# Optimization experiments

Hardware: AMD Instinct MI355X
Metric: run time of the kernel (lower is better)

## Reference

```python
import jax, jax.numpy as jnp
import numpy as np

B = 1024      # batch
E = 1024      # encoding_dim
OUT = 34      # 17 joints x 2 coords


def setup_inputs() -> dict:
    key = jax.random.key(0)
    ks = jax.random.split(key, 8)
    s = 0.02  # weight init scale
    return {
        "h": jax.random.normal(ks[0], (B, E), dtype=jnp.float32),
        "c": jax.random.normal(ks[1], (B, E), dtype=jnp.float32),
        "W_ih": jax.random.normal(ks[2], (4 * E, E), dtype=jnp.float32) * s,
        "W_hh": jax.random.normal(ks[3], (4 * E, E), dtype=jnp.float32) * s,
        "b_ih": jax.random.normal(ks[4], (4 * E,), dtype=jnp.float32) * s,
        "b_hh": jax.random.normal(ks[5], (4 * E,), dtype=jnp.float32) * s,
        "W_out": jax.random.normal(ks[6], (OUT, E), dtype=jnp.float32) * s,
        "b_out": jax.random.normal(ks[7], (OUT,), dtype=jnp.float32) * s,
        "future_preds": 10,
    }


def reference(h, c, W_ih, W_hh, b_ih, b_hh, W_out, b_out, future_preds):
    E_ = h.shape[1]
    start = jnp.zeros_like(h)  # zeros=True start token

    def step(carry, _):
        h_t, c_t, x = carry
        # LSTMCell: gates in PyTorch order i, f, g, o
        gates = x @ W_ih.T + b_ih + h_t @ W_hh.T + b_hh  # [B, 4E]
        i = jax.nn.sigmoid(gates[:, 0 * E_:1 * E_])
        f = jax.nn.sigmoid(gates[:, 1 * E_:2 * E_])
        g = jnp.tanh(gates[:, 2 * E_:3 * E_])
        o = jax.nn.sigmoid(gates[:, 3 * E_:4 * E_])
        c_new = f * c_t + i * g
        h_new = o * jnp.tanh(c_new)
        return (h_new, c_new, h_new), h_new

    _, hs = jax.lax.scan(step, (h, c, start), None, length=future_preds)
    # hs: [T, B, E] -> [B, T, E]
    preds = jnp.transpose(hs, (1, 0, 2))
    return preds @ W_out.T + b_out  # [B, T, 34]
```

## Files before the change

kernel.cpp:

```cpp
#include <hip/hip_runtime.h>
#include <cstdint>
#include <cstddef>

#define E_DIM   1024
#define B_DIM   1024
#define HPITCH  1040
#define T_STEPS 10
#define OUT_DIM 34
#define OUT_PAD 48
#define HSTR    24
#define QK      256
#define WQ_ELEMS (64 * QK)
#define DYN_LDS (2 * WQ_ELEMS * 2 + 128 * HSTR * 2)
#define HSLOT  ((size_t)B_DIM * HPITCH)

typedef __attribute__((ext_vector_type(4))) float  f32x4;
typedef __attribute__((ext_vector_type(8))) __bf16 bf16x8;

__device__ __forceinline__ unsigned short f2bf(float f) {
    unsigned int u = __float_as_uint(f);
    u = (u + 0x7FFFu + ((u >> 16) & 1u)) >> 16;
    return (unsigned short)u;
}
__device__ __forceinline__ float sigmoid_(float x) { return 1.0f / (1.0f + __expf(-x)); }
__device__ __forceinline__ float tanh_(float x)    { return 2.0f / (1.0f + __expf(-2.0f * x)) - 1.0f; }

__global__ void prep_weights_frag(const float* __restrict__ W_ih, const float* __restrict__ W_hh,
                                  unsigned short* __restrict__ WsumF, unsigned short* __restrict__ WhhF) {
    const int bn = blockIdx.x >> 3, qtr = (blockIdx.x >> 1) & 3, half = blockIdx.x & 1;
    const int nt = threadIdx.x >> 6, lane = threadIdx.x & 63;
    const int j = lane & 15, q = lane >> 4;
    const int srow = nt * E_DIM + bn * 16 + j;
    const float* wi = W_ih + (size_t)srow * E_DIM;
    const float* wh = W_hh + (size_t)srow * E_DIM;
    const size_t dstb = (size_t)bn * 65536 + (size_t)qtr * 16384 + nt * 512 + lane * 8;
#pragma unroll
    for (int ks8i = 0; ks8i < 4; ++ks8i) {
        const int ks8 = half * 4 + ks8i;
        const int k = qtr * 256 + ks8 * 32 + q * 8;
        float4 i0 = *(const float4*)(wi + k);
        float4 i1 = *(const float4*)(wi + k + 4);
        float4 h0 = *(const float4*)(wh + k);
        float4 h1 = *(const float4*)(wh + k + 4);
        unsigned short* ds = WsumF + dstb + ks8 * 2048;
        unsigned short* dh = WhhF  + dstb + ks8 * 2048;
        ds[0] = f2bf(i0.x + h0.x); ds[1] = f2bf(i0.y + h0.y);
        ds[2] = f2bf(i0.z + h0.z); ds[3] = f2bf(i0.w + h0.w);
        ds[4] = f2bf(i1.x + h1.x); ds[5] = f2bf(i1.y + h1.y);
        ds[6] = f2bf(i1.z + h1.z); ds[7] = f2bf(i1.w + h1.w);
        dh[0] = f2bf(h0.x); dh[1] = f2bf(h0.y); dh[2] = f2bf(h0.z); dh[3] = f2bf(h0.w);
        dh[4] = f2bf(h1.x); dh[5] = f2bf(h1.y); dh[6] = f2bf(h1.z); dh[7] = f2bf(h1.w);
    }
}

__global__ void prep_state(const float* __restrict__ h0, const float* __restrict__ c0,
                           const float* __restrict__ W_out,
                           const float* __restrict__ b_ih, const float* __restrict__ b_hh,
                           unsigned short* __restrict__ hbuf, unsigned short* __restrict__ Woutp,
                           float* __restrict__ bperm, float* __restrict__ C) {
    const int b = blockIdx.x;
    const int t = threadIdx.x;
    if (b < 1024) {
        const size_t src = ((size_t)b * 256 + t) * 4;
        float4 hv = *(const float4*)(h0 + src);
        const size_t i = (size_t)b * HPITCH + t * 4;
        hbuf[i + 0] = f2bf(hv.x);
        hbuf[i + 1] = f2bf(hv.y);
        hbuf[i + 2] = f2bf(hv.z);
        hbuf[i + 3] = f2bf(hv.w);
    } else if (b < 1072) {
        const int o = b - 1024;
        const int k = t * 4;
        float4 w = make_float4(0.f, 0.f, 0.f, 0.f);
        if (o < OUT_DIM) w = *(const float4*)(W_out + (size_t)o * E_DIM + k);
        const size_t dst = (size_t)o * E_DIM + k;
        Woutp[dst + 0] = f2bf(w.x);
        Woutp[dst + 1] = f2bf(w.y);
        Woutp[dst + 2] = f2bf(w.z);
        Woutp[dst + 3] = f2bf(w.w);
    } else if (b < 1088) {
        const int n = (b - 1072) * 256 + t;
        const int g = (n >> 4) & 3;
        const int e = ((n >> 6) << 4) | (n & 15);
        const int srow = g * E_DIM + e;
        bperm[n] = b_ih[srow] + b_hh[srow];
    } else {
        const int m = b - 1088;
        const int e0 = t * 4;
        float4 v = *(const float4*)(c0 + (size_t)m * E_DIM + e0);
        const int bm = m >> 7, wave = (m >> 5) & 3, mt = (m >> 4) & 1, q = (m >> 2) & 3, r = m & 3;
        const float vv[4] = {v.x, v.y, v.z, v.w};
#pragma unroll
        for (int ii = 0; ii < 4; ++ii) {
            const int e = e0 + ii;
            const int bn = e >> 4, jj = e & 15;
            const int lane = q * 16 + jj;
            C[(((size_t)(bn * 8 + bm) * 4 + wave) * 64 + lane) * 8 + mt * 4 + r] = vv[ii];
        }
    }
}

__global__ __launch_bounds__(256, 2) void lstm_step(
    const unsigned short* __restrict__ WF,
    const float* __restrict__ bp,
    const unsigned short* __restrict__ Hin,
    float* __restrict__ C,
    unsigned short* __restrict__ Hout)
{
    extern __shared__ __align__(16) unsigned short smem[];
    unsigned short* Wbuf0 = smem;
    unsigned short* Wbuf1 = smem + WQ_ELEMS;
    unsigned short* Ht    = smem + 2 * WQ_ELEMS;

    const int tid  = threadIdx.x;
    const int wave = tid >> 6;
    const int lane = tid & 63;
    const int bn = blockIdx.x;
    const int bm = blockIdx.y;
    const int j  = lane & 15;
    const int q  = lane >> 4;

    f32x4 acc[2][4];
#pragma unroll
    for (int a = 0; a < 2; ++a)
#pragma unroll
        for (int b = 0; b < 4; ++b) acc[a][b] = (f32x4){0.f, 0.f, 0.f, 0.f};

    const int nb = bn * 64 + j;
    const float bi = bp[nb +  0];
    const float bf = bp[nb + 16];
    const float bg = bp[nb + 32];
    const float bo = bp[nb + 48];
    const size_t cbase = (((size_t)(bn * 8 + bm) * 4 + wave) * 64 + lane) * 8;
    float4 cold0 = *(const float4*)(C + cbase);
    float4 cold1 = *(const float4*)(C + cbase + 4);

    const unsigned short* arow0 = Hin + (size_t)(bm * 128 + wave * 32 + j) * HPITCH + q * 8;
    const unsigned short* arow1 = arow0 + (size_t)16 * HPITCH;
    const unsigned short* wsrc  = WF + (size_t)bn * 65536;

    uint4 ra[8][2];
#pragma unroll
    for (int p = 0; p < 8; ++p) {
        ra[p][0] = *(const uint4*)(arow0 + p * 32);
        ra[p][1] = *(const uint4*)(arow1 + p * 32);
    }

    uint4 wreg[8];
#pragma unroll
    for (int i = 0; i < 8; ++i)
        wreg[i] = *(const uint4*)(wsrc + (i * 256 + tid) * 8);
#pragma unroll
    for (int i = 0; i < 8; ++i)
        *(uint4*)(Wbuf0 + (i * 256 + tid) * 8) = wreg[i];
    __syncthreads();

    for (int qtr = 0; qtr < 4; ++qtr) {
        if (qtr < 3) {
#pragma unroll
            for (int i = 0; i < 8; ++i)
                wreg[i] = *(const uint4*)(wsrc + (size_t)(qtr + 1) * WQ_ELEMS + (i * 256 + tid) * 8);
        }
        const unsigned short* wb = ((qtr & 1) ? Wbuf1 : Wbuf0) + lane * 8;
#pragma unroll
        for (int ks8 = 0; ks8 < 8; ++ks8) {
            const int ks = qtr * 8 + ks8;
            bf16x8 av0 = __builtin_bit_cast(bf16x8, ra[ks8][0]);
            bf16x8 av1 = __builtin_bit_cast(bf16x8, ra[ks8][1]);
            bf16x8 bv[4];
#pragma unroll
            for (int nt = 0; nt < 4; ++nt)
                bv[nt] = *(const bf16x8*)(wb + (ks8 * 4 + nt) * 512);
#pragma unroll
            for (int nt = 0; nt < 4; ++nt) {
                acc[0][nt] = __builtin_amdgcn_mfma_f32_16x16x32_bf16(av0, bv[nt], acc[0][nt], 0, 0, 0);
                acc[1][nt] = __builtin_amdgcn_mfma_f32_16x16x32_bf16(av1, bv[nt], acc[1][nt], 0, 0, 0);
            }
            if (ks < 24) {
                ra[ks8][0] = *(const uint4*)(arow0 + (ks + 8) * 32);
                ra[ks8][1] = *(const uint4*)(arow1 + (ks + 8) * 32);
            }
        }
        if (qtr < 3) {
            unsigned short* wn_ = ((qtr + 1) & 1) ? Wbuf1 : Wbuf0;
#pragma unroll
            for (int i = 0; i < 8; ++i)
                *(uint4*)(wn_ + (i * 256 + tid) * 8) = wreg[i];
            __syncthreads();
        }
    }

    float4 cnew[2];
    const float coldv[2][4] = {{cold0.x, cold0.y, cold0.z, cold0.w},
                               {cold1.x, cold1.y, cold1.z, cold1.w}};
#pragma unroll
    for (int mt = 0; mt < 2; ++mt) {
#pragma unroll
        for (int r = 0; r < 4; ++r) {
            const float iv = sigmoid_(acc[mt][0][r] + bi);
            const float fv = sigmoid_(acc[mt][1][r] + bf);
            const float gv = tanh_(acc[mt][2][r] + bg);
            const float ov = sigmoid_(acc[mt][3][r] + bo);
            const float cn = fv * coldv[mt][r] + iv * gv;
            cnew[mt][r] = cn;
            const int rowl = wave * 32 + mt * 16 + q * 4 + r;
            Ht[rowl * HSTR + j] = f2bf(ov * tanh_(cn));
        }
    }
    *(float4*)(C + cbase)     = cnew[0];
    *(float4*)(C + cbase + 4) = cnew[1];
    __syncthreads();

    {
        const int row = tid >> 1, part = tid & 1;
        uint4 v = *(const uint4*)(Ht + row * HSTR + part * 8);
        *(uint4*)(Hout + (size_t)(bm * 128 + row) * HPITCH + bn * 16 + part * 8) = v;
    }
}

__global__ __launch_bounds__(256) void proj_kernel(
    const unsigned short* __restrict__ Hs,
    const unsigned short* __restrict__ Wo,
    const float* __restrict__ b_out,
    float* __restrict__ Out)
{
    __shared__ float red[4][32][OUT_PAD];

    const int tid = threadIdx.x, wave = tid >> 6, lane = tid & 63;
    const int j = lane & 15, q = lane >> 4;
    const int t  = blockIdx.y;
    const int bb = blockIdx.x;
    const unsigned short* Hbase = Hs + (size_t)t * HSLOT + (size_t)bb * 32 * HPITCH;
    const int k0 = wave * 256;

    f32x4 acc[2][3];
#pragma unroll
    for (int a = 0; a < 2; ++a)
#pragma unroll
        for (int b = 0; b < 3; ++b) acc[a][b] = (f32x4){0.f, 0.f, 0.f, 0.f};

#pragma unroll
    for (int kk = 0; kk < 256; kk += 32) {
        const int kc = k0 + kk + q * 8;
        bf16x8 av[2], bv[3];
#pragma unroll
        for (int mt = 0; mt < 2; ++mt)
            av[mt] = *(const bf16x8*)(Hbase + (size_t)(mt * 16 + j) * HPITCH + kc);
#pragma unroll
        for (int nt = 0; nt < 3; ++nt)
            bv[nt] = *(const bf16x8*)(Wo + (size_t)(nt * 16 + j) * E_DIM + kc);
#pragma unroll
        for (int mt = 0; mt < 2; ++mt)
#pragma unroll
            for (int nt = 0; nt < 3; ++nt)
                acc[mt][nt] = __builtin_amdgcn_mfma_f32_16x16x32_bf16(av[mt], bv[nt], acc[mt][nt], 0, 0, 0);
    }

#pragma unroll
    for (int mt = 0; mt < 2; ++mt)
#pragma unroll
        for (int nt = 0; nt < 3; ++nt)
#pragma unroll
            for (int r = 0; r < 4; ++r)
                red[wave][mt * 16 + q * 4 + r][nt * 16 + j] = acc[mt][nt][r];
    __syncthreads();

#pragma unroll
    for (int ii = 0; ii < 6; ++ii) {
        const int idx = tid * 6 + ii;
        const int row = idx / OUT_PAD, o = idx % OUT_PAD;
        if (o < OUT_DIM) {
            const float s = red[0][row][o] + red[1][row][o] + red[2][row][o] + red[3][row][o];
            Out[((size_t)(bb * 32 + row) * T_STEPS + t) * OUT_DIM + o] = s + b_out[o];
        }
    }
}

extern "C" void kernel_launch(void* const* d_in, const int* in_sizes, int n_in,
                              void* d_out, int out_size, void* d_ws, size_t ws_size,
                              hipStream_t stream) {
    (void)in_sizes; (void)n_in; (void)out_size; (void)ws_size;
    const float* h     = (const float*)d_in[0];
    const float* c     = (const float*)d_in[1];
    const float* W_ih  = (const float*)d_in[2];
    const float* W_hh  = (const float*)d_in[3];
    const float* b_ih  = (const float*)d_in[4];
    const float* b_hh  = (const float*)d_in[5];
    const float* W_out = (const float*)d_in[6];
    const float* b_out = (const float*)d_in[7];
    float* out = (float*)d_out;

    char* ws = (char*)d_ws;
    unsigned short* WsumF = (unsigned short*)(ws + 0);
    unsigned short* WhhF  = (unsigned short*)(ws + 8388608);
    float*          bperm = (float*)(ws + 16777216);
    unsigned short* Woutp = (unsigned short*)(ws + 16842752);
    float*          cbuf  = (float*)(ws + 16941056);
    unsigned short* hs    = (unsigned short*)(ws + 21135360);

    hipFuncSetAttribute((const void*)lstm_step,
                        hipFuncAttributeMaxDynamicSharedMemorySize, DYN_LDS);

    prep_weights_frag<<<512, 256, 0, stream>>>(W_ih, W_hh, WsumF, WhhF);
    prep_state<<<2112, 256, 0, stream>>>(h, c, W_out, b_ih, b_hh, hs, Woutp, bperm, cbuf);

    lstm_step<<<dim3(64, 8), 256, DYN_LDS, stream>>>(WhhF, bperm, hs, cbuf, hs + HSLOT);
    for (int t = 1; t < T_STEPS; ++t)
        lstm_step<<<dim3(64, 8), 256, DYN_LDS, stream>>>(WsumF, bperm,
                                                         hs + (size_t)t * HSLOT,
                                                         cbuf,
                                                         hs + (size_t)(t + 1) * HSLOT);

    proj_kernel<<<dim3(32, T_STEPS), 256, 0, stream>>>(hs + HSLOT, Woutp, b_out, out);
}
```

Measured before the change: 284.0 us.

## Load full weight slice into LDS once per 512-thread block covering 256 rows

Each block now has 512 threads and covers 256 batch rows instead of 128, so the grid halves. The block loads the whole 64-column weight slice (128 KB bf16) into LDS once, replacing the quarter-wise double buffering with its per-quarter barriers. Each weight slice is now read from global memory by half as many blocks, and three syncs per block go away. In exchange LDS use per block rises to about 140 KB, the upfront load is no longer overlapped with MFMA work, and occupancy likely drops to one block per CU.

```diff
diff --git a/kernel.cpp b/kernel.cpp
--- a/kernel.cpp
+++ b/kernel.cpp
@@ -9,9 +9,9 @@
 #define OUT_DIM 34
 #define OUT_PAD 48
 #define HSTR    24
-#define QK      256
-#define WQ_ELEMS (64 * QK)
-#define DYN_LDS (2 * WQ_ELEMS * 2 + 128 * HSTR * 2)
+#define WSLICE  65536
+#define HT_ROWS 256
+#define DYN_LDS (WSLICE * 2 + HT_ROWS * HSTR * 2)
 #define HSLOT  ((size_t)B_DIM * HPITCH)
 
 typedef __attribute__((ext_vector_type(4))) float  f32x4;
@@ -100,7 +100,7 @@
     }
 }
 
-__global__ __launch_bounds__(256, 2) void lstm_step(
+__global__ __launch_bounds__(512, 2) void lstm_step(
     const unsigned short* __restrict__ WF,
     const float* __restrict__ bp,
     const unsigned short* __restrict__ Hin,
@@ -108,15 +108,14 @@
     unsigned short* __restrict__ Hout)
 {
     extern __shared__ __align__(16) unsigned short smem[];
-    unsigned short* Wbuf0 = smem;
-    unsigned short* Wbuf1 = smem + WQ_ELEMS;
-    unsigned short* Ht    = smem + 2 * WQ_ELEMS;
+    unsigned short* Wlds = smem;
+    unsigned short* Ht   = smem + WSLICE;
 
     const int tid  = threadIdx.x;
-    const int wave = tid >> 6;
+    const int w    = tid >> 6;
     const int lane = tid & 63;
     const int bn = blockIdx.x;
-    const int bm = blockIdx.y;
+    const int g  = blockIdx.y;
     const int j  = lane & 15;
     const int q  = lane >> 4;
 
@@ -131,13 +130,27 @@
     const float bf = bp[nb + 16];
     const float bg = bp[nb + 32];
     const float bo = bp[nb + 48];
-    const size_t cbase = (((size_t)(bn * 8 + bm) * 4 + wave) * 64 + lane) * 8;
+    const int obm = g * 2 + (w >> 2), owv = w & 3;
+    const size_t cbase = (((size_t)(bn * 8 + obm) * 4 + owv) * 64 + lane) * 8;
     float4 cold0 = *(const float4*)(C + cbase);
     float4 cold1 = *(const float4*)(C + cbase + 4);
 
-    const unsigned short* arow0 = Hin + (size_t)(bm * 128 + wave * 32 + j) * HPITCH + q * 8;
+    const unsigned short* arow0 = Hin + (size_t)(g * 256 + w * 32 + j) * HPITCH + q * 8;
     const unsigned short* arow1 = arow0 + (size_t)16 * HPITCH;
-    const unsigned short* wsrc  = WF + (size_t)bn * 65536;
+    const unsigned short* wsrc  = WF + (size_t)bn * WSLICE;
+
+    {
+        uint4 wreg[8];
+#pragma unroll
+        for (int r2 = 0; r2 < 2; ++r2) {
+#pragma unroll
+            for (int i = 0; i < 8; ++i)
+                wreg[i] = *(const uint4*)(wsrc + ((r2 * 8 + i) * 512 + tid) * 8);
+#pragma unroll
+            for (int i = 0; i < 8; ++i)
+                *(uint4*)(Wlds + ((r2 * 8 + i) * 512 + tid) * 8) = wreg[i];
+        }
+    }
 
     uint4 ra[8][2];
 #pragma unroll
@@ -145,23 +158,10 @@
         ra[p][0] = *(const uint4*)(arow0 + p * 32);
         ra[p][1] = *(const uint4*)(arow1 + p * 32);
     }
-
-    uint4 wreg[8];
-#pragma unroll
-    for (int i = 0; i < 8; ++i)
-        wreg[i] = *(const uint4*)(wsrc + (i * 256 + tid) * 8);
-#pragma unroll
-    for (int i = 0; i < 8; ++i)
-        *(uint4*)(Wbuf0 + (i * 256 + tid) * 8) = wreg[i];
     __syncthreads();
 
     for (int qtr = 0; qtr < 4; ++qtr) {
-        if (qtr < 3) {
-#pragma unroll
-            for (int i = 0; i < 8; ++i)
-                wreg[i] = *(const uint4*)(wsrc + (size_t)(qtr + 1) * WQ_ELEMS + (i * 256 + tid) * 8);
-        }
-        const unsigned short* wb = ((qtr & 1) ? Wbuf1 : Wbuf0) + lane * 8;
+        const unsigned short* wb = Wlds + qtr * 16384 + lane * 8;
 #pragma unroll
         for (int ks8 = 0; ks8 < 8; ++ks8) {
             const int ks = qtr * 8 + ks8;
@@ -181,13 +181,6 @@
                 ra[ks8][1] = *(const uint4*)(arow1 + (ks + 8) * 32);
             }
         }
-        if (qtr < 3) {
-            unsigned short* wn_ = ((qtr + 1) & 1) ? Wbuf1 : Wbuf0;
-#pragma unroll
-            for (int i = 0; i < 8; ++i)
-                *(uint4*)(wn_ + (i * 256 + tid) * 8) = wreg[i];
-            __syncthreads();
-        }
     }
 
     float4 cnew[2];
@@ -203,7 +196,7 @@
             const float ov = sigmoid_(acc[mt][3][r] + bo);
             const float cn = fv * coldv[mt][r] + iv * gv;
             cnew[mt][r] = cn;
-            const int rowl = wave * 32 + mt * 16 + q * 4 + r;
+            const int rowl = w * 32 + mt * 16 + q * 4 + r;
             Ht[rowl * HSTR + j] = f2bf(ov * tanh_(cn));
         }
     }
@@ -214,7 +207,7 @@
     {
         const int row = tid >> 1, part = tid & 1;
         uint4 v = *(const uint4*)(Ht + row * HSTR + part * 8);
-        *(uint4*)(Hout + (size_t)(bm * 128 + row) * HPITCH + bn * 16 + part * 8) = v;
+        *(uint4*)(Hout + (size_t)(g * 256 + row) * HPITCH + bn * 16 + part * 8) = v;
     }
 }
 
@@ -304,9 +297,9 @@
     prep_weights_frag<<<512, 256, 0, stream>>>(W_ih, W_hh, WsumF, WhhF);
     prep_state<<<2112, 256, 0, stream>>>(h, c, W_out, b_ih, b_hh, hs, Woutp, bperm, cbuf);
 
-    lstm_step<<<dim3(64, 8), 256, DYN_LDS, stream>>>(WhhF, bperm, hs, cbuf, hs + HSLOT);
+    lstm_step<<<dim3(64, 4), 512, DYN_LDS, stream>>>(WhhF, bperm, hs, cbuf, hs + HSLOT);
     for (int t = 1; t < T_STEPS; ++t)
-        lstm_step<<<dim3(64, 8), 256, DYN_LDS, stream>>>(WsumF, bperm,
+        lstm_step<<<dim3(64, 4), 512, DYN_LDS, stream>>>(WsumF, bperm,
                                                          hs + (size_t)t * HSLOT,
                                                          cbuf,
                                                          hs + (size_t)(t + 1) * HSLOT);
```

After: 275.6 us. 1.03x faster.
